# Kernel tuning notes

Measured on AMD Instinct MI355X. Metric: run time of the kernel, lower is better.

## Reference

```python
import jax, jax.numpy as jnp
import numpy as np

DMODEL = 1024
NHEAD = 16
DHEAD = DMODEL // NHEAD

def _layernorm(x, g, b, eps=1e-5):
    mu = jnp.mean(x, axis=-1, keepdims=True)
    var = jnp.var(x, axis=-1, keepdims=True)
    return (x - mu) * jax.lax.rsqrt(var + eps) * g + b

def setup_inputs() -> dict:
    key = jax.random.key(0)
    ks = jax.random.split(key, 12)
    b, lq, lv, d = 2, 2048, 2048, DMODEL
    s = 1.0 / np.sqrt(d)
    return {
        "q": jax.random.normal(ks[0], (b, lq, d), jnp.float32),
        "k": jax.random.normal(ks[1], (b, lv, d), jnp.float32),
        "v": jax.random.normal(ks[2], (b, lv, d), jnp.float32),
        "qln_g": jnp.ones((d,), jnp.float32),
        "qln_b": jnp.zeros((d,), jnp.float32),
        "kvln_g": jnp.ones((d,), jnp.float32),
        "kvln_b": jnp.zeros((d,), jnp.float32),
        "Wq": jax.random.normal(ks[3], (d, d), jnp.float32) * s,
        "Wk": jax.random.normal(ks[4], (d, d), jnp.float32) * s,
        "Wv": jax.random.normal(ks[5], (d, d), jnp.float32) * s,
        "Wg": jax.random.normal(ks[6], (d, d), jnp.float32) * s,
        "bg": jnp.zeros((d,), jnp.float32),
        "Wo": jax.random.normal(ks[7], (d, d), jnp.float32) * s,
    }

def reference(q, k, v, qln_g, qln_b, kvln_g, kvln_b, Wq, Wk, Wv, Wg, bg, Wo):
    b, lq, d = q.shape
    lv = v.shape[1]
    qn = _layernorm(q, qln_g, qln_b)           # [b, lq, d]
    q_ = qn @ Wq.T
    kk = _layernorm(k, kvln_g, kvln_b) @ Wk.T
    vv = _layernorm(v, kvln_g, kvln_b) @ Wv.T
    qh = q_.reshape(b, lq, NHEAD, DHEAD)       # bqhd
    kh = kk.reshape(b, lv, NHEAD, DHEAD)
    vh = vv.reshape(b, lv, NHEAD, DHEAD)
    scores = jnp.einsum('bqhd,bkhd->bhqk', qh, kh) / np.sqrt(DHEAD)
    attn = jax.nn.softmax(scores, axis=-1)
    y = jnp.einsum('bhqk,bkhd->bqhd', attn, vh).reshape(b, lq, d)
    g = jax.nn.sigmoid(qn @ Wg.T + bg)
    return (y * g) @ Wo.T
```

## Files before the change

### kernel.cpp

```cpp
#include <hip/hip_runtime.h>
#include <hip/hip_bf16.h>

#define DMODEL 1024
#define NHEAD  16
#define DHEAD  64
#define BATCH  2
#define LQ     2048
#define LV     2048
#define ROWS   (BATCH*LQ)
#define WELEMS (DMODEL*DMODEL)
#define BH     (BATCH*NHEAD)

typedef short bf16x8 __attribute__((ext_vector_type(8)));
typedef float f32x4  __attribute__((ext_vector_type(4)));

__device__ __forceinline__ float bf2f(unsigned short s) {
    union { unsigned u; float f; } v; v.u = ((unsigned)s) << 16;
    return v.f;
}
__device__ __forceinline__ unsigned pk_bf(float a, float b) {
    union { __hip_bfloat162 h; unsigned u; } c;
    c.h = __float22bfloat162_rn(make_float2(a, b));
    return c.u;
}

__device__ __forceinline__ void cp16_g2l(const void* g, void* l) {
    __builtin_amdgcn_global_load_lds(
        (const __attribute__((address_space(1))) void*)g,
        (__attribute__((address_space(3))) void*)l,
        16, 0, 0);
}

#define QSCALE (0.125f * 1.4426950408889634f)

__global__ __launch_bounds__(256) void prep_kernel(
    const float* q, const float* k, const float* v,
    const float* qg, const float* qb, const float* kvg, const float* kvb,
    const float* Wq, const float* Wk, const float* Wv, const float* Wg, const float* Wo,
    unsigned short* qn, unsigned short* kn, unsigned short* vn, unsigned short* wb)
{
    __shared__ float rs[4], rq[4];
    int z = blockIdx.y;
    if (z < 5) {
        if (blockIdx.x >= WELEMS / 1024) return;
        const float* srcs[5] = {Wq, Wk, Wv, Wg, Wo};
        const float* s = srcs[z];
        unsigned short* d = wb + (size_t)z * WELEMS;
        int i = (blockIdx.x * 256 + threadIdx.x) * 4;
        float4 x = *(const float4*)(s + i);
        uint2 o = make_uint2(pk_bf(x.x, x.y), pk_bf(x.z, x.w));
        *(uint2*)(d + i) = o;
        return;
    }
    int row = blockIdx.x;
    const float *x, *gp, *bp; unsigned short* o;
    if      (z == 5) { x = q; gp = qg;  bp = qb;  o = qn; }
    else if (z == 6) { x = k; gp = kvg; bp = kvb; o = kn; }
    else             { x = v; gp = kvg; bp = kvb; o = vn; }

    int col = threadIdx.x * 4;
    float4 xv = *(const float4*)(x + (size_t)row * DMODEL + col);
    float s  = xv.x + xv.y + xv.z + xv.w;
    float sq = xv.x*xv.x + xv.y*xv.y + xv.z*xv.z + xv.w*xv.w;
    #pragma unroll
    for (int off = 1; off < 64; off <<= 1) { s += __shfl_xor(s, off); sq += __shfl_xor(sq, off); }

    int wave = threadIdx.x >> 6, lane = threadIdx.x & 63;
    if (lane == 0) { rs[wave] = s; rq[wave] = sq; }
    __syncthreads();
    float ts = rs[0] + rs[1] + rs[2] + rs[3];
    float tq = rq[0] + rq[1] + rq[2] + rq[3];
    float mu  = ts * (1.0f / DMODEL);
    float var = tq * (1.0f / DMODEL) - mu * mu;
    float inv = rsqrtf(var + 1e-5f);

    float4 gv = *(const float4*)(gp + col);
    float4 bv = *(const float4*)(bp + col);
    float r0 = (xv.x - mu) * inv * gv.x + bv.x;
    float r1 = (xv.y - mu) * inv * gv.y + bv.y;
    float r2 = (xv.z - mu) * inv * gv.z + bv.z;
    float r3 = (xv.w - mu) * inv * gv.w + bv.w;
    *(uint2*)(o + (size_t)row * DMODEL + col) = make_uint2(pk_bf(r0, r1), pk_bf(r2, r3));
}

template<int MODE>
__device__ __forceinline__ void gemm256_core(
    const unsigned short* A, const unsigned short* Bw,
    unsigned short* Obf, const float* bias, float scale,
    unsigned short* Al, unsigned short* Bl, int bm, int bn)
{
    int tid  = threadIdx.x;
    int w = tid >> 6, l = tid & 63, quad = l >> 4, L = l & 15;
    int wm = w >> 2, wn = w & 3;

    int c16 = (l & 7) ^ (l >> 3);
    const unsigned short* gAs = A  + (size_t)(bm * 256 + w * 8 + (l >> 3)) * DMODEL + c16 * 8;
    const unsigned short* gBs = Bw + (size_t)(bn * 256 + w * 8 + (l >> 3)) * DMODEL + c16 * 8;
    int dstE = w * 512;

    #define STG_A2(t, ro) do { const unsigned short* s_ = gAs + (size_t)(ro) * DMODEL + (t) * 64; \
        unsigned short* d_ = Al + ((t) & 1) * 16384 + (ro) * 64 + dstE;                           \
        cp16_g2l(s_, d_); cp16_g2l(s_ + 64 * DMODEL, d_ + 4096); } while (0)
    #define STG_B2(t, ro) do { const unsigned short* s_ = gBs + (size_t)(ro) * DMODEL + (t) * 64; \
        unsigned short* d_ = Bl + ((t) & 1) * 16384 + (ro) * 64 + dstE;                           \
        cp16_g2l(s_, d_); cp16_g2l(s_ + 64 * DMODEL, d_ + 4096); } while (0)

    int sw = (L & 7) << 3;
    int o0 = (quad * 8) ^ sw;
    int o1 = (32 + quad * 8) ^ sw;

    f32x4 acc[8][4];
    #pragma unroll
    for (int i = 0; i < 8; ++i)
        #pragma unroll
        for (int j = 0; j < 4; ++j) acc[i][j] = (f32x4){0.f, 0.f, 0.f, 0.f};

    STG_A2(0, 0); STG_A2(0, 128); STG_B2(0, 0); STG_B2(0, 128);
    STG_A2(1, 0); STG_A2(1, 128);
    asm volatile("s_waitcnt vmcnt(4)" ::: "memory");
    __builtin_amdgcn_s_barrier();

    const int NT = DMODEL / 64;
    for (int t = 0; t < NT; ++t) {
        const unsigned short* Ab = Al + (t & 1) * 16384 + wm * 8192;
        const unsigned short* Bb = Bl + (t & 1) * 16384 + wn * 4096;
        bf16x8 b0[4], b1[4], a0[2], a1[2], r0v[6], r1v[6];

        #pragma unroll
        for (int j = 0; j < 4; ++j) {
            b0[j] = *(const bf16x8*)&Bb[(j * 16 + L) * 64 + o0];
            b1[j] = *(const bf16x8*)&Bb[(j * 16 + L) * 64 + o1];
        }
        #pragma unroll
        for (int i2 = 0; i2 < 2; ++i2) {
            a0[i2] = *(const bf16x8*)&Ab[(i2 * 16 + L) * 64 + o0];
            a1[i2] = *(const bf16x8*)&Ab[(i2 * 16 + L) * 64 + o1];
        }
        if (t + 1 < NT) STG_B2(t + 1, 0);
        __builtin_amdgcn_s_barrier();
        __builtin_amdgcn_s_setprio(1);
        #pragma unroll
        for (int i2 = 0; i2 < 2; ++i2)
            #pragma unroll
            for (int j = 0; j < 4; ++j) {
                if (MODE == 3) {
                    acc[i2][j] = __builtin_amdgcn_mfma_f32_16x16x32_bf16(a0[i2], b0[j], acc[i2][j], 0, 0, 0);
                    acc[i2][j] = __builtin_amdgcn_mfma_f32_16x16x32_bf16(a1[i2], b1[j], acc[i2][j], 0, 0, 0);
                } else {
                    acc[i2][j] = __builtin_amdgcn_mfma_f32_16x16x32_bf16(b0[j], a0[i2], acc[i2][j], 0, 0, 0);
                    acc[i2][j] = __builtin_amdgcn_mfma_f32_16x16x32_bf16(b1[j], a1[i2], acc[i2][j], 0, 0, 0);
                }
            }
        __builtin_amdgcn_s_setprio(0);
        __builtin_amdgcn_s_barrier();

        #pragma unroll
        for (int r = 0; r < 6; ++r) {
            r0v[r] = *(const bf16x8*)&Ab[((32 + r * 16) + L) * 64 + o0];
            r1v[r] = *(const bf16x8*)&Ab[((32 + r * 16) + L) * 64 + o1];
        }
        if (t + 1 < NT) STG_B2(t + 1, 128);
        __builtin_amdgcn_s_barrier();
        __builtin_amdgcn_s_setprio(1);
        #pragma unroll
        for (int i2 = 0; i2 < 2; ++i2)
            #pragma unroll
            for (int j = 0; j < 4; ++j) {
                if (MODE == 3) {
                    acc[2 + i2][j] = __builtin_amdgcn_mfma_f32_16x16x32_bf16(r0v[i2], b0[j], acc[2 + i2][j], 0, 0, 0);
                    acc[2 + i2][j] = __builtin_amdgcn_mfma_f32_16x16x32_bf16(r1v[i2], b1[j], acc[2 + i2][j], 0, 0, 0);
                } else {
                    acc[2 + i2][j] = __builtin_amdgcn_mfma_f32_16x16x32_bf16(b0[j], r0v[i2], acc[2 + i2][j], 0, 0, 0);
                    acc[2 + i2][j] = __builtin_amdgcn_mfma_f32_16x16x32_bf16(b1[j], r1v[i2], acc[2 + i2][j], 0, 0, 0);
                }
            }
        __builtin_amdgcn_s_setprio(0);
        asm volatile("s_waitcnt lgkmcnt(0)" ::: "memory");
        __builtin_amdgcn_sched_barrier(0);
        __builtin_amdgcn_s_barrier();

        if (t + 2 < NT) { STG_A2(t + 2, 0); STG_A2(t + 2, 128); }
        __builtin_amdgcn_s_barrier();
        __builtin_amdgcn_s_setprio(1);
        #pragma unroll
        for (int i2 = 0; i2 < 4; ++i2)
            #pragma unroll
            for (int j = 0; j < 4; ++j) {
                if (MODE == 3) {
                    acc[4 + i2][j] = __builtin_amdgcn_mfma_f32_16x16x32_bf16(r0v[2 + i2], b0[j], acc[4 + i2][j], 0, 0, 0);
                    acc[4 + i2][j] = __builtin_amdgcn_mfma_f32_16x16x32_bf16(r1v[2 + i2], b1[j], acc[4 + i2][j], 0, 0, 0);
                } else {
                    acc[4 + i2][j] = __builtin_amdgcn_mfma_f32_16x16x32_bf16(b0[j], r0v[2 + i2], acc[4 + i2][j], 0, 0, 0);
                    acc[4 + i2][j] = __builtin_amdgcn_mfma_f32_16x16x32_bf16(b1[j], r1v[2 + i2], acc[4 + i2][j], 0, 0, 0);
                }
            }
        __builtin_amdgcn_s_setprio(0);
        if (t + 2 < NT) asm volatile("s_waitcnt vmcnt(4)" ::: "memory");
        else            asm volatile("s_waitcnt vmcnt(0)" ::: "memory");
        __builtin_amdgcn_s_barrier();
    }
    #undef STG_A2
    #undef STG_B2

    #pragma unroll
    for (int i = 0; i < 8; ++i) {
        #pragma unroll
        for (int j = 0; j < 4; ++j) {
            f32x4 a = acc[i][j];
            if (MODE == 3) {
                int gcol  = bn * 256 + wn * 64 + j * 16 + L;
                int grow0 = bm * 256 + wm * 128 + i * 16 + quad * 4;
                int b = grow0 >> 11, key0 = grow0 & 2047;
                int h = gcol >> 6,   dd   = gcol & 63;
                uint2 o = make_uint2(pk_bf(a[0], a[1]), pk_bf(a[2], a[3]));
                *(uint2*)&Obf[(((size_t)(b * NHEAD + h) * DHEAD + dd) << 11) + key0] = o;
            } else {
                int grow  = bm * 256 + wm * 128 + i * 16 + L;
                int gcol0 = bn * 256 + wn * 64 + j * 16 + quad * 4;
                size_t idx = (size_t)grow * DMODEL + gcol0;
                if (MODE == 0) {
                    uint2 o = make_uint2(pk_bf(a[0] * scale, a[1] * scale),
                                         pk_bf(a[2] * scale, a[3] * scale));
                    *(uint2*)&Obf[idx] = o;
                } else {
                    float4 bv = *(const float4*)&bias[gcol0];
                    float s0 = 1.0f / (1.0f + __expf(-(a[0] + bv.x)));
                    float s1 = 1.0f / (1.0f + __expf(-(a[1] + bv.y)));
                    float s2 = 1.0f / (1.0f + __expf(-(a[2] + bv.z)));
                    float s3 = 1.0f / (1.0f + __expf(-(a[3] + bv.w)));
                    *(uint2*)&Obf[idx] = make_uint2(pk_bf(s0, s1), pk_bf(s2, s3));
                }
            }
        }
    }
}

__global__ __launch_bounds__(512, 2) void gemm256_kernel(
    const unsigned short* qn, const unsigned short* kn, const unsigned short* vn,
    const unsigned short* wb,
    unsigned short* qs, unsigned short* kkp, unsigned short* vt, unsigned short* gate,
    const float* bg)
{
    __shared__ __align__(16) unsigned short Al[2 * 256 * 64];
    __shared__ __align__(16) unsigned short Bl[2 * 256 * 64];
    int f = blockIdx.x, xcd = f & 7, s = f >> 3;
    int z  = xcd & 3;
    int bm = ((xcd >> 2) << 3) | (s >> 2);
    int bn = s & 3;
    switch (z) {
        case 0:  gemm256_core<0>(qn, wb + 0 * WELEMS, qs,   nullptr, QSCALE, Al, Bl, bm, bn); break;
        case 1:  gemm256_core<0>(kn, wb + 1 * WELEMS, kkp,  nullptr, 1.0f,   Al, Bl, bm, bn); break;
        case 2:  gemm256_core<3>(vn, wb + 2 * WELEMS, vt,   nullptr, 1.0f,   Al, Bl, bm, bn); break;
        default: gemm256_core<1>(qn, wb + 3 * WELEMS, gate, bg,      1.0f,   Al, Bl, bm, bn); break;
    }
}

template<int MODE>
__device__ __forceinline__ void gemm_bt_core(
    const unsigned short* A, const unsigned short* Bw,
    unsigned short* Obf, float* Of32, const float* bias, float scale,
    unsigned short* Al, unsigned short* Bl, int bm, int bn)
{
    int tid  = threadIdx.x;
    int wave = tid >> 6, lane = tid & 63, quad = lane >> 4, L = lane & 15;
    int wm = wave >> 1, wn = wave & 1;

    int srow = wave * 16 + (lane >> 2);
    int scol = (lane & 3) * 8;
    const unsigned short* gA = A  + (size_t)(bm * 128 + srow) * DMODEL + scol;
    const unsigned short* gB = Bw + (size_t)(bn * 128 + srow) * DMODEL + scol;
    int lofs0 = wave * 16 * 32;
    int lofs1 = (64 + wave * 16) * 32;

    f32x4 acc[4][4];
    #pragma unroll
    for (int i = 0; i < 4; ++i)
        #pragma unroll
        for (int j = 0; j < 4; ++j) acc[i][j] = (f32x4){0.f, 0.f, 0.f, 0.f};

    cp16_g2l(gA,               Al + lofs0);
    cp16_g2l(gA + 64 * DMODEL, Al + lofs1);
    cp16_g2l(gB,               Bl + lofs0);
    cp16_g2l(gB + 64 * DMODEL, Bl + lofs1);

    int buf = 0;
    for (int k0 = 0; k0 < DMODEL; k0 += 32, buf ^= 1) {
        __syncthreads();
        if (k0 + 32 < DMODEL) {
            int nb = (buf ^ 1) * (128 * 32);
            cp16_g2l(gA + k0 + 32,               Al + nb + lofs0);
            cp16_g2l(gA + 64 * DMODEL + k0 + 32, Al + nb + lofs1);
            cp16_g2l(gB + k0 + 32,               Bl + nb + lofs0);
            cp16_g2l(gB + 64 * DMODEL + k0 + 32, Bl + nb + lofs1);
        }
        const unsigned short* Ab = Al + buf * (128 * 32);
        const unsigned short* Bb = Bl + buf * (128 * 32);
        bf16x8 af[4], bfr[4];
        #pragma unroll
        for (int i = 0; i < 4; ++i)
            af[i] = *(const bf16x8*)&Ab[(wm * 64 + i * 16 + L) * 32 + quad * 8];
        #pragma unroll
        for (int j = 0; j < 4; ++j)
            bfr[j] = *(const bf16x8*)&Bb[(wn * 64 + j * 16 + L) * 32 + quad * 8];
        #pragma unroll
        for (int i = 0; i < 4; ++i)
            #pragma unroll
            for (int j = 0; j < 4; ++j) {
                if (MODE == 3)
                    acc[i][j] = __builtin_amdgcn_mfma_f32_16x16x32_bf16(af[i], bfr[j], acc[i][j], 0, 0, 0);
                else
                    acc[i][j] = __builtin_amdgcn_mfma_f32_16x16x32_bf16(bfr[j], af[i], acc[i][j], 0, 0, 0);
            }
    }

    #pragma unroll
    for (int i = 0; i < 4; ++i) {
        #pragma unroll
        for (int j = 0; j < 4; ++j) {
            f32x4 a = acc[i][j];
            int grow  = bm * 128 + wm * 64 + i * 16 + L;
            int gcol0 = bn * 128 + wn * 64 + j * 16 + quad * 4;
            size_t idx = (size_t)grow * DMODEL + gcol0;
            if (MODE == 2) {
                *(f32x4*)&Of32[idx] = a;
            } else if (MODE == 0) {
                uint2 o = make_uint2(pk_bf(a[0] * scale, a[1] * scale),
                                     pk_bf(a[2] * scale, a[3] * scale));
                *(uint2*)&Obf[idx] = o;
            }
        }
    }
}

__device__ __forceinline__ void xcd_map(int& bm, int& bn) {
    int f = blockIdx.y * 8 + blockIdx.x;
    int xcd = f & 7, s = f >> 3;
    bn = s & 7;
    bm = ((s >> 3) << 3) | xcd;
}

__global__ __launch_bounds__(256) void gemm_f32out_kernel(
    const unsigned short* A, const unsigned short* Bw, float* O)
{
    __shared__ __align__(16) unsigned short Al[2 * 128 * 32];
    __shared__ __align__(16) unsigned short Bl[2 * 128 * 32];
    int bm, bn; xcd_map(bm, bn);
    gemm_bt_core<2>(A, Bw, nullptr, O, nullptr, 1.0f, Al, Bl, bm, bn);
}

__global__ __launch_bounds__(256, 4) void attn_kernel(
    const unsigned short* qs, const unsigned short* kk, const unsigned short* vt,
    const unsigned short* gate, unsigned short* yg)
{
    __shared__ __align__(16) unsigned short Kl[2 * 64 * 64];
    __shared__ __align__(16) unsigned short Vl[2 * 64 * 64];

    int tid  = threadIdx.x;
    int wave = tid >> 6, lane = tid & 63, quad = lane >> 4, L = lane & 15;

    int f  = blockIdx.y * 32 + blockIdx.x;
    int bh = (f & 7) * 4 + ((f >> 3) & 3);
    int qt = f >> 5;
    int bb = bh >> 4, h = bh & 15;
    int q0 = qt * 64;

    const unsigned short* Qb =
        qs + ((size_t)(bb * LQ + q0 + wave * 16 + L)) * DMODEL + h * DHEAD;
    bf16x8 aq0 = *(const bf16x8*)(Qb + quad * 8);
    bf16x8 aq1 = *(const bf16x8*)(Qb + 32 + quad * 8);

    f32x4 acc[4];
    #pragma unroll
    for (int nt = 0; nt < 4; ++nt) acc[nt] = (f32x4){0.f, 0.f, 0.f, 0.f};
    f32x4 lacc = (f32x4){0.f, 0.f, 0.f, 0.f};
    bf16x8 ones;
    #pragma unroll
    for (int j = 0; j < 8; ++j) ones[j] = (short)0x3F80;

    int rloc = lane >> 3;
    int c16  = (lane & 7) ^ rloc;
    int key0 = (wave & 1) * 32 + (rloc >> 2) * 8 + (wave >> 1) * 4 + (rloc & 3);

    const unsigned short* gK = kk + (size_t)bb * LV * DMODEL + h * DHEAD
                                  + (size_t)key0 * DMODEL + c16 * 8;
    const unsigned short* gV = vt + ((size_t)((bb * NHEAD + h) * DHEAD
                                  + wave * 16 + rloc)) * LV + c16 * 8;
    char* KlB = (char*)Kl;
    char* VlB = (char*)Vl;
    int dst0 = wave * 2048;

    cp16_g2l(gK,               KlB + dst0);
    cp16_g2l(gK + 16 * DMODEL, KlB + dst0 + 1024);
    cp16_g2l(gV,               VlB + dst0);
    cp16_g2l(gV + 8 * LV,      VlB + dst0 + 1024);

    int sl0 = (quad ^ (L & 7)) * 8;
    int buf = 0;
    for (int it = 0; it < LV / 64; ++it, buf ^= 1) {
        __syncthreads();
        if (it + 1 < LV / 64) {
            gK += 64 * DMODEL; gV += 64;
            int nb = (buf ^ 1) * 8192 + dst0;
            cp16_g2l(gK,               KlB + nb);
            cp16_g2l(gK + 16 * DMODEL, KlB + nb + 1024);
            cp16_g2l(gV,               VlB + nb);
            cp16_g2l(gV + 8 * LV,      VlB + nb + 1024);
        }
        const unsigned short* Kb = Kl + buf * 4096;
        const unsigned short* Vb = Vl + buf * 4096;

        f32x4 zz[4];
        __builtin_amdgcn_s_setprio(1);
        #pragma unroll
        for (int kt = 0; kt < 4; ++kt) {
            bf16x8 bk0 = *(const bf16x8*)&Kb[(kt * 16 + L) * 64 + sl0];
            bf16x8 bk1 = *(const bf16x8*)&Kb[(kt * 16 + L) * 64 + (sl0 ^ 32)];
            f32x4 z = (f32x4){0.f, 0.f, 0.f, 0.f};
            z = __builtin_amdgcn_mfma_f32_16x16x32_bf16(bk0, aq0, z, 0, 0, 0);
            z = __builtin_amdgcn_mfma_f32_16x16x32_bf16(bk1, aq1, z, 0, 0, 0);
            zz[kt] = z;
        }
        __builtin_amdgcn_s_setprio(0);

        union { unsigned u[4]; bf16x8 h; } pa0, pa1;
        pa0.u[0] = pk_bf(__builtin_amdgcn_exp2f(zz[0][0]), __builtin_amdgcn_exp2f(zz[0][1]));
        pa0.u[1] = pk_bf(__builtin_amdgcn_exp2f(zz[0][2]), __builtin_amdgcn_exp2f(zz[0][3]));
        pa0.u[2] = pk_bf(__builtin_amdgcn_exp2f(zz[2][0]), __builtin_amdgcn_exp2f(zz[2][1]));
        pa0.u[3] = pk_bf(__builtin_amdgcn_exp2f(zz[2][2]), __builtin_amdgcn_exp2f(zz[2][3]));
        pa1.u[0] = pk_bf(__builtin_amdgcn_exp2f(zz[1][0]), __builtin_amdgcn_exp2f(zz[1][1]));
        pa1.u[1] = pk_bf(__builtin_amdgcn_exp2f(zz[1][2]), __builtin_amdgcn_exp2f(zz[1][3]));
        pa1.u[2] = pk_bf(__builtin_amdgcn_exp2f(zz[3][0]), __builtin_amdgcn_exp2f(zz[3][1]));
        pa1.u[3] = pk_bf(__builtin_amdgcn_exp2f(zz[3][2]), __builtin_amdgcn_exp2f(zz[3][3]));

        __builtin_amdgcn_s_setprio(1);
        lacc = __builtin_amdgcn_mfma_f32_16x16x32_bf16(ones, pa0.h, lacc, 0, 0, 0);
        lacc = __builtin_amdgcn_mfma_f32_16x16x32_bf16(ones, pa1.h, lacc, 0, 0, 0);
        #pragma unroll
        for (int nt = 0; nt < 4; ++nt) {
            bf16x8 vb0 = *(const bf16x8*)&Vb[(nt * 16 + L) * 64 + sl0];
            bf16x8 vb1 = *(const bf16x8*)&Vb[(nt * 16 + L) * 64 + (sl0 ^ 32)];
            acc[nt] = __builtin_amdgcn_mfma_f32_16x16x32_bf16(vb0, pa0.h, acc[nt], 0, 0, 0);
            acc[nt] = __builtin_amdgcn_mfma_f32_16x16x32_bf16(vb1, pa1.h, acc[nt], 0, 0, 0);
        }
        __builtin_amdgcn_s_setprio(0);
    }

    float inv_l = 1.0f / lacc[0];
    size_t rb = ((size_t)(bb * LQ + q0 + wave * 16 + L)) * DMODEL + h * DHEAD;
    #pragma unroll
    for (int nt = 0; nt < 4; ++nt) {
        size_t idx = rb + nt * 16 + quad * 4;
        ushort4 g = *(const ushort4*)&gate[idx];
        float y0 = acc[nt][0] * inv_l * bf2f(g.x);
        float y1 = acc[nt][1] * inv_l * bf2f(g.y);
        float y2 = acc[nt][2] * inv_l * bf2f(g.z);
        float y3 = acc[nt][3] * inv_l * bf2f(g.w);
        *(uint2*)&yg[idx] = make_uint2(pk_bf(y0, y1), pk_bf(y2, y3));
    }
}

extern "C" void kernel_launch(void* const* d_in, const int* in_sizes, int n_in,
                              void* d_out, int out_size, void* d_ws, size_t ws_size,
                              hipStream_t stream)
{
    const float* q      = (const float*)d_in[0];
    const float* k      = (const float*)d_in[1];
    const float* v      = (const float*)d_in[2];
    const float* qln_g  = (const float*)d_in[3];
    const float* qln_b  = (const float*)d_in[4];
    const float* kvln_g = (const float*)d_in[5];
    const float* kvln_b = (const float*)d_in[6];
    const float* Wq     = (const float*)d_in[7];
    const float* Wk     = (const float*)d_in[8];
    const float* Wv     = (const float*)d_in[9];
    const float* Wg     = (const float*)d_in[10];
    const float* bg     = (const float*)d_in[11];
    const float* Wo     = (const float*)d_in[12];
    float* out = (float*)d_out;

    const size_t T8 = (size_t)ROWS * DMODEL * 2;
    char* ws = (char*)d_ws;
    unsigned short* qn   = (unsigned short*)(ws + 0 * T8);
    unsigned short* kn   = (unsigned short*)(ws + 1 * T8);
    unsigned short* vn   = (unsigned short*)(ws + 2 * T8);
    unsigned short* qs   = (unsigned short*)(ws + 3 * T8);
    unsigned short* kkp  = (unsigned short*)(ws + 4 * T8);
    unsigned short* vt   = (unsigned short*)(ws + 5 * T8);
    unsigned short* gate = (unsigned short*)(ws + 6 * T8);
    unsigned short* yg   = (unsigned short*)(ws + 7 * T8);
    unsigned short* wb   = (unsigned short*)(ws + 8 * T8);

    prep_kernel<<<dim3(ROWS, 8), 256, 0, stream>>>(
        q, k, v, qln_g, qln_b, kvln_g, kvln_b, Wq, Wk, Wv, Wg, Wo, qn, kn, vn, wb);
    gemm256_kernel<<<dim3(256), 512, 0, stream>>>(
        qn, kn, vn, wb, qs, kkp, vt, gate, bg);
    attn_kernel<<<dim3(32, 32), 256, 0, stream>>>(qs, kkp, vt, gate, yg);
    gemm_f32out_kernel<<<dim3(DMODEL / 128, ROWS / 128), 256, 0, stream>>>(yg, wb + 4 * WELEMS, out);
}
```

Baseline: 234.2 us.

## Software-pipeline attention loop: overlap PV of previous tile with QK of current

Restructures the attention main loop so the exp/softmax-weight result of tile t-1 is consumed by the PV MFMAs while tile t's QK MFMAs run, with a prologue and epilogue. V tiles move to a triple-buffered LDS ring so the previous tile's V stays resident while new tiles load. It also hoists all LDS fragment loads ahead of the MFMA block. The aim is to hide exp/convert latency and LDS read latency behind matrix work. It costs more registers and LDS, which may pressure occupancy at four blocks per CU.

```diff
diff --git a/kernel.cpp b/kernel.cpp
--- a/kernel.cpp
+++ b/kernel.cpp
@@ -353,7 +353,7 @@
     const unsigned short* gate, unsigned short* yg)
 {
     __shared__ __align__(16) unsigned short Kl[2 * 64 * 64];
-    __shared__ __align__(16) unsigned short Vl[2 * 64 * 64];
+    __shared__ __align__(16) unsigned short Vl[3 * 64 * 64];
 
     int tid  = threadIdx.x;
     int wave = tid >> 6, lane = tid & 63, quad = lane >> 4, L = lane & 15;
@@ -389,26 +389,23 @@
     char* VlB = (char*)Vl;
     int dst0 = wave * 2048;
 
+    int sl0 = (quad ^ (L & 7)) * 8;
+
     cp16_g2l(gK,               KlB + dst0);
     cp16_g2l(gK + 16 * DMODEL, KlB + dst0 + 1024);
     cp16_g2l(gV,               VlB + dst0);
     cp16_g2l(gV + 8 * LV,      VlB + dst0 + 1024);
-
-    int sl0 = (quad ^ (L & 7)) * 8;
-    int buf = 0;
-    for (int it = 0; it < LV / 64; ++it, buf ^= 1) {
-        __syncthreads();
-        if (it + 1 < LV / 64) {
-            gK += 64 * DMODEL; gV += 64;
-            int nb = (buf ^ 1) * 8192 + dst0;
-            cp16_g2l(gK,               KlB + nb);
-            cp16_g2l(gK + 16 * DMODEL, KlB + nb + 1024);
-            cp16_g2l(gV,               VlB + nb);
-            cp16_g2l(gV + 8 * LV,      VlB + nb + 1024);
-        }
-        const unsigned short* Kb = Kl + buf * 4096;
-        const unsigned short* Vb = Vl + buf * 4096;
-
+    __syncthreads();
+    gK += 64 * DMODEL; gV += 64;
+    cp16_g2l(gK,               KlB + 8192 + dst0);
+    cp16_g2l(gK + 16 * DMODEL, KlB + 8192 + dst0 + 1024);
+    cp16_g2l(gV,               VlB + 8192 + dst0);
+    cp16_g2l(gV + 8 * LV,      VlB + 8192 + dst0 + 1024);
+
+    bf16x8 pap0, pap1;
+
+    {
+        const unsigned short* Kb = Kl;
         f32x4 zz[4];
         __builtin_amdgcn_s_setprio(1);
         #pragma unroll
@@ -421,7 +418,6 @@
             zz[kt] = z;
         }
         __builtin_amdgcn_s_setprio(0);
-
         union { unsigned u[4]; bf16x8 h; } pa0, pa1;
         pa0.u[0] = pk_bf(__builtin_amdgcn_exp2f(zz[0][0]), __builtin_amdgcn_exp2f(zz[0][1]));
         pa0.u[1] = pk_bf(__builtin_amdgcn_exp2f(zz[0][2]), __builtin_amdgcn_exp2f(zz[0][3]));
@@ -431,18 +427,85 @@
         pa1.u[1] = pk_bf(__builtin_amdgcn_exp2f(zz[1][2]), __builtin_amdgcn_exp2f(zz[1][3]));
         pa1.u[2] = pk_bf(__builtin_amdgcn_exp2f(zz[3][0]), __builtin_amdgcn_exp2f(zz[3][1]));
         pa1.u[3] = pk_bf(__builtin_amdgcn_exp2f(zz[3][2]), __builtin_amdgcn_exp2f(zz[3][3]));
+        pap0 = pa0.h; pap1 = pa1.h;
+    }
+
+    const int NT = LV / 64;
+    int vs = 2;
+    int vr = 0;
+    for (int t = 1; t < NT; ++t) {
+        __syncthreads();
+        if (t + 1 < NT) {
+            gK += 64 * DMODEL; gV += 64;
+            int kb = ((t + 1) & 1) * 8192;
+            cp16_g2l(gK,               KlB + kb + dst0);
+            cp16_g2l(gK + 16 * DMODEL, KlB + kb + dst0 + 1024);
+            int vb_ = vs * 8192;
+            cp16_g2l(gV,               VlB + vb_ + dst0);
+            cp16_g2l(gV + 8 * LV,      VlB + vb_ + dst0 + 1024);
+            vs = (vs == 2) ? 0 : vs + 1;
+        }
+        const unsigned short* Vb = Vl + vr * 4096;
+        vr = (vr == 2) ? 0 : vr + 1;
+        const unsigned short* Kb = Kl + (t & 1) * 4096;
+
+        bf16x8 vf0[4], vf1[4];
+        #pragma unroll
+        for (int nt = 0; nt < 4; ++nt) {
+            vf0[nt] = *(const bf16x8*)&Vb[(nt * 16 + L) * 64 + sl0];
+            vf1[nt] = *(const bf16x8*)&Vb[(nt * 16 + L) * 64 + (sl0 ^ 32)];
+        }
+        bf16x8 kf0[4], kf1[4];
+        #pragma unroll
+        for (int kt = 0; kt < 4; ++kt) {
+            kf0[kt] = *(const bf16x8*)&Kb[(kt * 16 + L) * 64 + sl0];
+            kf1[kt] = *(const bf16x8*)&Kb[(kt * 16 + L) * 64 + (sl0 ^ 32)];
+        }
 
         __builtin_amdgcn_s_setprio(1);
-        lacc = __builtin_amdgcn_mfma_f32_16x16x32_bf16(ones, pa0.h, lacc, 0, 0, 0);
-        lacc = __builtin_amdgcn_mfma_f32_16x16x32_bf16(ones, pa1.h, lacc, 0, 0, 0);
+        lacc = __builtin_amdgcn_mfma_f32_16x16x32_bf16(ones, pap0, lacc, 0, 0, 0);
+        lacc = __builtin_amdgcn_mfma_f32_16x16x32_bf16(ones, pap1, lacc, 0, 0, 0);
         #pragma unroll
         for (int nt = 0; nt < 4; ++nt) {
-            bf16x8 vb0 = *(const bf16x8*)&Vb[(nt * 16 + L) * 64 + sl0];
-            bf16x8 vb1 = *(const bf16x8*)&Vb[(nt * 16 + L) * 64 + (sl0 ^ 32)];
-            acc[nt] = __builtin_amdgcn_mfma_f32_16x16x32_bf16(vb0, pa0.h, acc[nt], 0, 0, 0);
-            acc[nt] = __builtin_amdgcn_mfma_f32_16x16x32_bf16(vb1, pa1.h, acc[nt], 0, 0, 0);
+            acc[nt] = __builtin_amdgcn_mfma_f32_16x16x32_bf16(vf0[nt], pap0, acc[nt], 0, 0, 0);
+            acc[nt] = __builtin_amdgcn_mfma_f32_16x16x32_bf16(vf1[nt], pap1, acc[nt], 0, 0, 0);
+        }
+        f32x4 zz[4];
+        #pragma unroll
+        for (int kt = 0; kt < 4; ++kt) {
+            f32x4 z = (f32x4){0.f, 0.f, 0.f, 0.f};
+            z = __builtin_amdgcn_mfma_f32_16x16x32_bf16(kf0[kt], aq0, z, 0, 0, 0);
+            z = __builtin_amdgcn_mfma_f32_16x16x32_bf16(kf1[kt], aq1, z, 0, 0, 0);
+            zz[kt] = z;
         }
         __builtin_amdgcn_s_setprio(0);
+        union { unsigned u[4]; bf16x8 h; } pa0, pa1;
+        pa0.u[0] = pk_bf(__builtin_amdgcn_exp2f(zz[0][0]), __builtin_amdgcn_exp2f(zz[0][1]));
+        pa0.u[1] = pk_bf(__builtin_amdgcn_exp2f(zz[0][2]), __builtin_amdgcn_exp2f(zz[0][3]));
+        pa0.u[2] = pk_bf(__builtin_amdgcn_exp2f(zz[2][0]), __builtin_amdgcn_exp2f(zz[2][1]));
+        pa0.u[3] = pk_bf(__builtin_amdgcn_exp2f(zz[2][2]), __builtin_amdgcn_exp2f(zz[2][3]));
+        pa1.u[0] = pk_bf(__builtin_amdgcn_exp2f(zz[1][0]), __builtin_amdgcn_exp2f(zz[1][1]));
+        pa1.u[1] = pk_bf(__builtin_amdgcn_exp2f(zz[1][2]), __builtin_amdgcn_exp2f(zz[1][3]));
+        pa1.u[2] = pk_bf(__builtin_amdgcn_exp2f(zz[3][0]), __builtin_amdgcn_exp2f(zz[3][1]));
+        pa1.u[3] = pk_bf(__builtin_amdgcn_exp2f(zz[3][2]), __builtin_amdgcn_exp2f(zz[3][3]));
+        pap0 = pa0.h; pap1 = pa1.h;
+    }
+
+    {
+        const unsigned short* Vb = Vl + 1 * 4096;
+        bf16x8 vf0[4], vf1[4];
+        #pragma unroll
+        for (int nt = 0; nt < 4; ++nt) {
+            vf0[nt] = *(const bf16x8*)&Vb[(nt * 16 + L) * 64 + sl0];
+            vf1[nt] = *(const bf16x8*)&Vb[(nt * 16 + L) * 64 + (sl0 ^ 32)];
+        }
+        lacc = __builtin_amdgcn_mfma_f32_16x16x32_bf16(ones, pap0, lacc, 0, 0, 0);
+        lacc = __builtin_amdgcn_mfma_f32_16x16x32_bf16(ones, pap1, lacc, 0, 0, 0);
+        #pragma unroll
+        for (int nt = 0; nt < 4; ++nt) {
+            acc[nt] = __builtin_amdgcn_mfma_f32_16x16x32_bf16(vf0[nt], pap0, acc[nt], 0, 0, 0);
+            acc[nt] = __builtin_amdgcn_mfma_f32_16x16x32_bf16(vf1[nt], pap1, acc[nt], 0, 0, 0);
+        }
     }
 
     float inv_l = 1.0f / lacc[0];
```

Result: faster. 227.9 us (-2.7%).
